# Kernel tuning notes

Measured on AMD Instinct MI355X. Metric: run time of the kernel, lower is better.

## Reference

```python
import jax, jax.numpy as jnp
import numpy as np

B, N, E, H, ET = 1, 50000, 600000, 128, 8
EPS = 1e-5


def setup_inputs() -> dict:
    key = jax.random.key(0)
    ks = jax.random.split(key, 20)
    s = 1.0 / np.sqrt(H)
    s2 = 1.0 / np.sqrt(2 * H)
    u = lambda k, shape, b: jax.random.uniform(k, shape, jnp.float32, -b, b)
    return {
        "hidden": jax.random.normal(ks[0], (B, N, H), jnp.float32),
        "edge_index": jax.random.randint(ks[1], (2, E), 0, N),
        "edge_type": jax.random.randint(ks[2], (E,), 0, ET),
        "edge_emb": jax.random.normal(ks[3], (ET, H), jnp.float32),
        "Wq": u(ks[4], (H, H), s), "bq": u(ks[5], (H,), s),
        "Wk": u(ks[6], (H, H), s), "bk": u(ks[7], (H,), s),
        "Wv": u(ks[8], (H, H), s), "bv": u(ks[9], (H,), s),
        "Web": u(ks[10], (H, 1), s), "beb": u(ks[11], (1,), s),
        "W1": u(ks[12], (2 * H, H), s2), "b1": u(ks[13], (H,), s2),
        "W2": u(ks[14], (H, H), s), "b2": u(ks[15], (H,), s),
        "gamma": jnp.ones((H,), jnp.float32),
        "beta": jnp.zeros((H,), jnp.float32),
    }


def reference(hidden, edge_index, edge_type, edge_emb, Wq, bq, Wk, bk, Wv, bv,
              Web, beb, W1, b1, W2, b2, gamma, beta):
    source, target = edge_index[0], edge_index[1]
    src_h = hidden[:, source]                      # [B,E,H] gather
    tgt_h = hidden[:, target]                      # [B,E,H] gather
    eh = edge_emb[edge_type]                       # [E,H]

    q = tgt_h @ Wq + bq                            # [B,E,H]
    sk = src_h + eh[None]                          # [B,E,H]
    k = sk @ Wk + bk
    v = sk @ Wv + bv

    logits = (q * k).sum(-1) / np.sqrt(H)          # [B,E]
    logits = logits + (eh @ Web + beb)[:, 0][None] # edge bias, same across batch

    # segment softmax over incoming edges per target node
    lt = logits.T                                  # [E,B]
    mx = jax.ops.segment_max(lt, target, num_segments=N)   # [N,B]
    ex = jnp.exp(lt - mx[target])
    sm = jax.ops.segment_sum(ex, target, num_segments=N)   # [N,B]
    w = (ex / sm[target]).T                        # [B,E]

    messages = v * w[..., None]                    # [B,E,H]
    agg = jax.ops.segment_sum(jnp.moveaxis(messages, 1, 0), target,
                              num_segments=N)      # [N,B,H]
    agg = jnp.moveaxis(agg, 0, 1)                  # [B,N,H]

    h = jnp.concatenate([hidden, agg], axis=-1)    # [B,N,2H]
    upd = jax.nn.silu(h @ W1 + b1) @ W2 + b2

    x = hidden + upd
    mu = x.mean(-1, keepdims=True)
    var = ((x - mu) ** 2).mean(-1, keepdims=True)
    return (x - mu) / jnp.sqrt(var + EPS) * gamma + beta
```

## Files before the change

### kernel.cpp

```cpp
#include <hip/hip_runtime.h>
#include <math.h>

#define NN 50000
#define NPAD 50048
#define NTILES 3128
#define NE 600000
#define H 128
#define ET 8
#define EPS 1e-5f
#define INVSQ 0.08838834764831845f

typedef __attribute__((ext_vector_type(8))) short bf16x8;
typedef __attribute__((ext_vector_type(8))) unsigned short u16x8;
typedef __attribute__((ext_vector_type(4))) float f32x4;

static __device__ inline float bf_lo(unsigned int w) { return __uint_as_float(w << 16); }
static __device__ inline float bf_hi(unsigned int w) { return __uint_as_float(w & 0xFFFF0000u); }
static __device__ inline float bfu(unsigned short v) {
  return __uint_as_float((unsigned int)v << 16);
}
static __device__ inline unsigned short f2bf(float f) {
  unsigned int u = __float_as_uint(f);
  return (unsigned short)((u + 0x7FFFu + ((u >> 16) & 1u)) >> 16);
}

#define PH_B 3125
#define PW_B 384
#define ET_B 8
#define HIST_B 2344

__global__ __launch_bounds__(256) void prep_all_kernel(
    const float* __restrict__ hidden, const float* __restrict__ edge_emb,
    const float* __restrict__ Wq, const float* __restrict__ Wk, const float* __restrict__ Wv,
    const float* __restrict__ W1, const float* __restrict__ W2,
    const float* __restrict__ Web, const float* __restrict__ beb,
    const int* __restrict__ tgt,
    unsigned short* __restrict__ hcat, unsigned short* __restrict__ WqkvT,
    unsigned short* __restrict__ W1T, unsigned short* __restrict__ W2T,
    unsigned short* __restrict__ KefTT, float* __restrict__ Vef, float* __restrict__ ebuf,
    int* __restrict__ deg) {
  const int blk = blockIdx.x;
  const int t = threadIdx.x;
  if (blk < PH_B) {
    int g = blk * 256 + t;
    int row = g >> 4, seg = g & 15;
    const float4* src = (const float4*)(hidden + (size_t)row * 128 + seg * 8);
    float4 x0 = src[0], x1 = src[1];
    u16x8 o;
    o[0] = f2bf(x0.x); o[1] = f2bf(x0.y); o[2] = f2bf(x0.z); o[3] = f2bf(x0.w);
    o[4] = f2bf(x1.x); o[5] = f2bf(x1.y); o[6] = f2bf(x1.z); o[7] = f2bf(x1.w);
    *(u16x8*)(hcat + (size_t)row * 256 + seg * 8) = o;
  } else if (blk < PH_B + PW_B) {
    int idx = (blk - PH_B) * 256 + t;
    if (idx < 49152) {
      int r = idx >> 7, k = idx & 127;
      const float* W = (r < 128) ? Wq : (r < 256) ? Wk : Wv;
      WqkvT[idx] = f2bf(W[k * 128 + (r & 127)]);
    } else if (idx < 81920) {
      int j = idx - 49152;
      int r = j >> 8, k = j & 255;
      W1T[j] = f2bf(W1[k * 128 + r]);
    } else if (idx < 98304) {
      int j = idx - 81920;
      int r = j >> 7, k = j & 127;
      W2T[j] = f2bf(W2[k * 128 + r]);
    }
  } else if (blk < PH_B + PW_B + ET_B) {
    int e = blk - (PH_B + PW_B);
    if (t < 128) {
      float sk = 0.f, sv = 0.f;
      for (int i = 0; i < 128; ++i) {
        float ev = edge_emb[e * 128 + i];
        sk = fmaf(ev, Wk[i * 128 + t], sk);
        sv = fmaf(ev, Wv[i * 128 + t], sv);
      }
      KefTT[e * 128 + t] = f2bf(sk);
      KefTT[(e + 8) * 128 + t] = 0;
      Vef[e * 128 + t] = sv;
    } else if (t == 128) {
      float s2 = beb[0];
      for (int i = 0; i < 128; ++i) s2 = fmaf(edge_emb[e * 128 + i], Web[i], s2);
      ebuf[e] = s2;
    }
  } else {
    int e = (blk - (PH_B + PW_B + ET_B)) * 256 + t;
    if (e < NE) atomicAdd(&deg[tgt[e]], 1);
  }
}

__global__ __launch_bounds__(512) void qkv_mfma_kernel(
    const unsigned short* __restrict__ hcat, const unsigned short* __restrict__ WqkvT,
    const float* __restrict__ bq, const float* __restrict__ bk, const float* __restrict__ bv,
    const unsigned short* __restrict__ KefTT, const float* __restrict__ ebuf,
    unsigned short* __restrict__ Qb, unsigned short* __restrict__ KV_u16,
    float* __restrict__ qke) {
  __shared__ unsigned short stage[64][392];
  const int tid = threadIdx.x;
  const int w = tid >> 6, l = tid & 63;
  const int wr = w >> 2, wc = w & 3;
  const int lr = l & 15, lg = l >> 4;
  const int blk = blockIdx.x;

  f32x4 acc[2][6] = {};
  const unsigned short* Ab = hcat + (size_t)(blk * 64 + wr * 32 + lr) * 256 + lg * 8;
  const unsigned short* Bb = WqkvT + (size_t)(wc * 96 + lr) * 128 + lg * 8;
#pragma unroll
  for (int ks = 0; ks < 4; ++ks) {
    bf16x8 a0 = *(const bf16x8*)(Ab + ks * 32);
    bf16x8 a1 = *(const bf16x8*)(Ab + 16 * 256 + ks * 32);
#pragma unroll
    for (int ct = 0; ct < 6; ++ct) {
      bf16x8 b = *(const bf16x8*)(Bb + ct * 16 * 128 + ks * 32);
      acc[0][ct] = __builtin_amdgcn_mfma_f32_16x16x32_bf16(a0, b, acc[0][ct], 0, 0, 0);
      acc[1][ct] = __builtin_amdgcn_mfma_f32_16x16x32_bf16(a1, b, acc[1][ct], 0, 0, 0);
    }
  }
#pragma unroll
  for (int ct = 0; ct < 6; ++ct) {
    int c = wc * 96 + ct * 16 + lr;
    float bias = (c < 128) ? bq[c] : (c < 256) ? bk[c - 128] : bv[c - 256];
    float sc = (c < 128) ? INVSQ : 1.f;
    int off;
    if (c < 128) off = c;
    else if (c < 256) { int j = c - 128; off = 128 + ((j >> 1) << 2) + (j & 1); }
    else { int j = c - 256; off = 128 + ((j >> 1) << 2) + 2 + (j & 1); }
#pragma unroll
    for (int mt = 0; mt < 2; ++mt)
#pragma unroll
      for (int j = 0; j < 4; ++j)
        stage[wr * 32 + mt * 16 + lg * 4 + j][off] = f2bf((acc[mt][ct][j] + bias) * sc);
  }
  __syncthreads();
  for (int idx = tid; idx < 64 * 48; idx += 512) {
    int r = idx / 48, g = idx % 48;
    int row = blk * 64 + r;
    if (row >= NN) continue;
    u16x8 v = *(const u16x8*)(&stage[r][g * 8]);
    if (g < 16) *(u16x8*)(Qb + (size_t)row * 128 + g * 8) = v;
    else *(u16x8*)(KV_u16 + (size_t)row * 256 + (g - 16) * 8) = v;
  }
  if (w < 4) {
    f32x4 aq = {0.f, 0.f, 0.f, 0.f};
    const unsigned short* qrow = &stage[w * 16 + lr][0];
    const unsigned short* brow = KefTT + lr * 128;
#pragma unroll
    for (int ks = 0; ks < 4; ++ks) {
      bf16x8 af = *(const bf16x8*)(qrow + lg * 8 + ks * 32);
      bf16x8 bf = *(const bf16x8*)(brow + lg * 8 + ks * 32);
      aq = __builtin_amdgcn_mfma_f32_16x16x32_bf16(af, bf, aq, 0, 0, 0);
    }
    if (lr < 8) {
      float ebv = ebuf[lr];
#pragma unroll
      for (int j = 0; j < 4; ++j) {
        int node = blk * 64 + w * 16 + lg * 4 + j;
        if (node < NN) qke[(size_t)node * 8 + lr] = aq[j] + ebv;
      }
    }
  }
}

__global__ __launch_bounds__(256) void scan1_kernel(const int* __restrict__ deg,
                                                    int* __restrict__ excl,
                                                    int* __restrict__ sums) {
  __shared__ int buf[256];
  int idx = blockIdx.x * 256 + threadIdx.x;
  int v = (idx < NN) ? deg[idx] : 0;
  buf[threadIdx.x] = v;
  __syncthreads();
  for (int o = 1; o < 256; o <<= 1) {
    int tv = (threadIdx.x >= o) ? buf[threadIdx.x - o] : 0;
    __syncthreads();
    buf[threadIdx.x] += tv;
    __syncthreads();
  }
  if (idx < NN) excl[idx] = buf[threadIdx.x] - v;
  if (threadIdx.x == 255) sums[blockIdx.x] = buf[255];
}

__global__ __launch_bounds__(256) void scan2_kernel(int* __restrict__ sums, int nb) {
  __shared__ int buf[256];
  int v = (threadIdx.x < nb) ? sums[threadIdx.x] : 0;
  buf[threadIdx.x] = v;
  __syncthreads();
  for (int o = 1; o < 256; o <<= 1) {
    int tv = (threadIdx.x >= o) ? buf[threadIdx.x - o] : 0;
    __syncthreads();
    buf[threadIdx.x] += tv;
    __syncthreads();
  }
  if (threadIdx.x < nb) sums[threadIdx.x] = buf[threadIdx.x] - v;
}

__global__ __launch_bounds__(256) void scan3_kernel(const int* __restrict__ excl,
                                                    const int* __restrict__ sums,
                                                    int* __restrict__ row_off,
                                                    int* __restrict__ cursor) {
  int idx = blockIdx.x * 256 + threadIdx.x;
  if (idx < NN) {
    int r = excl[idx] + sums[blockIdx.x];
    row_off[idx] = r;
    cursor[idx] = r;
  }
  if (idx == 0) row_off[NN] = NE;
}

__global__ void scatter_kernel(const int* __restrict__ src, const int* __restrict__ tgt,
                               const int* __restrict__ et, int* __restrict__ cursor,
                               int* __restrict__ packed) {
  int e = blockIdx.x * blockDim.x + threadIdx.x;
  if (e < NE) {
    int pos = atomicAdd(&cursor[tgt[e]], 1);
    packed[pos] = src[e] | (et[e] << 16);
  }
}

__global__ __launch_bounds__(256) void attn_kernel(
    const unsigned short* __restrict__ Qb, const uint4* __restrict__ KV4,
    const float* __restrict__ qke, const float* __restrict__ Vef,
    const int* __restrict__ row_off, const int* __restrict__ packed,
    unsigned short* __restrict__ hcat_u16) {
  const int wid = (blockIdx.x * blockDim.x + threadIdx.x) >> 6;
  const int lane = threadIdx.x & 63;
  const int g = lane >> 4, m = lane & 15;
  const int beg = row_off[wid], end = row_off[wid + 1];
  u16x8 qv = *(const u16x8*)(Qb + (size_t)wid * 128 + m * 8);
  float q[8];
#pragma unroll
  for (int j = 0; j < 8; ++j) q[j] = bfu(qv[j]);
  const float* qkb = qke + (size_t)wid * 8;
  float a[8] = {0.f, 0.f, 0.f, 0.f, 0.f, 0.f, 0.f, 0.f};
  float s = 0.f;
  for (int i = beg; i < end; i += 8) {
    int iA = i + g, iB = i + 4 + g;
    bool vA = iA < end, vB = iB < end;
    int pA = packed[vA ? iA : beg];
    int pB = packed[vB ? iB : beg];
    int sA = pA & 0xFFFF, eA = pA >> 16;
    int sB = pB & 0xFFFF, eB = pB >> 16;
    const uint4* rowA = KV4 + (size_t)sA * 32 + m * 2;
    const uint4* rowB = KV4 + (size_t)sB * 32 + m * 2;
    uint4 xA0 = rowA[0], xA1 = rowA[1];
    uint4 xB0 = rowB[0], xB1 = rowB[1];
    float dA, dB;
    dA = bf_lo(xA0.x) * q[0];
    dB = bf_lo(xB0.x) * q[0];
    dA = fmaf(bf_hi(xA0.x), q[1], dA);
    dB = fmaf(bf_hi(xB0.x), q[1], dB);
    dA = fmaf(bf_lo(xA0.z), q[2], dA);
    dB = fmaf(bf_lo(xB0.z), q[2], dB);
    dA = fmaf(bf_hi(xA0.z), q[3], dA);
    dB = fmaf(bf_hi(xB0.z), q[3], dB);
    dA = fmaf(bf_lo(xA1.x), q[4], dA);
    dB = fmaf(bf_lo(xB1.x), q[4], dB);
    dA = fmaf(bf_hi(xA1.x), q[5], dA);
    dB = fmaf(bf_hi(xB1.x), q[5], dB);
    dA = fmaf(bf_lo(xA1.z), q[6], dA);
    dB = fmaf(bf_lo(xB1.z), q[6], dB);
    dA = fmaf(bf_hi(xA1.z), q[7], dA);
    dB = fmaf(bf_hi(xB1.z), q[7], dB);
#pragma unroll
    for (int o = 8; o >= 1; o >>= 1) {
      dA += __shfl_xor(dA, o);
      dB += __shfl_xor(dB, o);
    }
    float peA = __expf(dA + qkb[eA]);
    float peB = __expf(dB + qkb[eB]);
    peA = vA ? peA : 0.f;
    peB = vB ? peB : 0.f;
    s += peA + peB;
    const float4* vefA = (const float4*)(Vef + eA * 128 + m * 8);
    const float4* vefB = (const float4*)(Vef + eB * 128 + m * 8);
    float4 vA0 = vefA[0], vA1 = vefA[1];
    float4 vB0 = vefB[0], vB1 = vefB[1];
    a[0] = fmaf(peA, bf_lo(xA0.y) + vA0.x, a[0]);
    a[1] = fmaf(peA, bf_hi(xA0.y) + vA0.y, a[1]);
    a[2] = fmaf(peA, bf_lo(xA0.w) + vA0.z, a[2]);
    a[3] = fmaf(peA, bf_hi(xA0.w) + vA0.w, a[3]);
    a[4] = fmaf(peA, bf_lo(xA1.y) + vA1.x, a[4]);
    a[5] = fmaf(peA, bf_hi(xA1.y) + vA1.y, a[5]);
    a[6] = fmaf(peA, bf_lo(xA1.w) + vA1.z, a[6]);
    a[7] = fmaf(peA, bf_hi(xA1.w) + vA1.w, a[7]);
    a[0] = fmaf(peB, bf_lo(xB0.y) + vB0.x, a[0]);
    a[1] = fmaf(peB, bf_hi(xB0.y) + vB0.y, a[1]);
    a[2] = fmaf(peB, bf_lo(xB0.w) + vB0.z, a[2]);
    a[3] = fmaf(peB, bf_hi(xB0.w) + vB0.w, a[3]);
    a[4] = fmaf(peB, bf_lo(xB1.y) + vB1.x, a[4]);
    a[5] = fmaf(peB, bf_hi(xB1.y) + vB1.y, a[5]);
    a[6] = fmaf(peB, bf_lo(xB1.w) + vB1.z, a[6]);
    a[7] = fmaf(peB, bf_hi(xB1.w) + vB1.w, a[7]);
  }
#pragma unroll
  for (int o = 16; o <= 32; o <<= 1) {
    s += __shfl_xor(s, o);
#pragma unroll
    for (int j = 0; j < 8; ++j) a[j] += __shfl_xor(a[j], o);
  }
  if (g == 0) {
    float inv = (s > 0.f) ? 1.f / s : 0.f;
    u16x8 o;
#pragma unroll
    for (int j = 0; j < 8; ++j) o[j] = f2bf(a[j] * inv);
    *(u16x8*)(hcat_u16 + (size_t)wid * 256 + 128 + m * 8) = o;
  }
}

__global__ __launch_bounds__(512) void ffn_mfma_kernel(
    const unsigned short* __restrict__ hcat, const float* __restrict__ hidden,
    const unsigned short* __restrict__ W1T, const unsigned short* __restrict__ W2T,
    const float* __restrict__ b1, const float* __restrict__ b2,
    const float* __restrict__ gamma, const float* __restrict__ beta,
    float* __restrict__ out) {
  __shared__ unsigned short w1s[32768];
  __shared__ unsigned short w2s[16384];
  __shared__ unsigned short mids[8][2176];
  const int tid = threadIdx.x;
  const int w = tid >> 6, l = tid & 63;
  const int lr = l & 15, lg = l >> 4;

#pragma unroll
  for (int it = 0; it < 8; ++it) {
    int idx = it * 512 + tid;
    int c = idx >> 5, ks8 = idx & 31;
    u16x8 v = *(const u16x8*)(W1T + c * 256 + ks8 * 8);
    int byte = (c * 512 + ks8 * 16) ^ ((c & 7) << 4);
    *(u16x8*)((char*)w1s + byte) = v;
  }
#pragma unroll
  for (int it = 0; it < 4; ++it) {
    int idx = it * 512 + tid;
    int c = idx >> 4, ks8 = idx & 15;
    u16x8 v = *(const u16x8*)(W2T + c * 128 + ks8 * 8);
    int byte = (c * 256 + ks8 * 16) ^ ((c & 7) << 4);
    *(u16x8*)((char*)w2s + byte) = v;
  }
  __syncthreads();

  float bias1[8], bias2[8], ga[8], be[8];
#pragma unroll
  for (int ct = 0; ct < 8; ++ct) {
    int c = ct * 16 + lr;
    bias1[ct] = b1[c];
    bias2[ct] = b2[c];
    ga[ct] = gamma[c];
    be[ct] = beta[c];
  }
  unsigned short* midw = mids[w];
  const char* w1b = (const char*)w1s;
  const char* w2b = (const char*)w2s;

  for (int t = blockIdx.x * 8 + w; t < NTILES; t += 2048) {
    const unsigned short* Ab = hcat + (size_t)(t * 16 + lr) * 256 + lg * 8;
    bf16x8 a[8];
#pragma unroll
    for (int ks = 0; ks < 8; ++ks) a[ks] = *(const bf16x8*)(Ab + ks * 32);

    f32x4 acc[8] = {};
#pragma unroll
    for (int ks = 0; ks < 8; ++ks) {
#pragma unroll
      for (int ct = 0; ct < 8; ++ct) {
        int byte = ((ct * 16 + lr) * 512 + (lg * 8 + ks * 32) * 2) ^ ((lr & 7) << 4);
        bf16x8 b = *(const bf16x8*)(w1b + byte);
        acc[ct] = __builtin_amdgcn_mfma_f32_16x16x32_bf16(a[ks], b, acc[ct], 0, 0, 0);
      }
    }

    float res[8][4];
#pragma unroll
    for (int ct = 0; ct < 8; ++ct)
#pragma unroll
      for (int j = 0; j < 4; ++j) {
        int r = t * 16 + lg * 4 + j;
        res[ct][j] = (r < NN) ? hidden[(size_t)r * 128 + ct * 16 + lr] : 0.f;
      }

#pragma unroll
    for (int ct = 0; ct < 8; ++ct) {
      float bb = bias1[ct];
#pragma unroll
      for (int j = 0; j < 4; ++j) {
        float x = acc[ct][j] + bb;
        float sl = x / (1.f + __expf(-x));
        midw[(lg * 4 + j) * 136 + ct * 16 + lr] = f2bf(sl);
      }
    }
    asm volatile("s_waitcnt lgkmcnt(0)" ::: "memory");
    __builtin_amdgcn_sched_barrier(0);

    f32x4 acc2[8] = {};
#pragma unroll
    for (int ks = 0; ks < 4; ++ks) {
      bf16x8 a2 = *(const bf16x8*)(midw + lr * 136 + lg * 8 + ks * 32);
#pragma unroll
      for (int ct = 0; ct < 8; ++ct) {
        int byte = ((ct * 16 + lr) * 256 + (lg * 8 + ks * 32) * 2) ^ ((lr & 7) << 4);
        bf16x8 b = *(const bf16x8*)(w2b + byte);
        acc2[ct] = __builtin_amdgcn_mfma_f32_16x16x32_bf16(a2, b, acc2[ct], 0, 0, 0);
      }
    }

    float x[8][4];
#pragma unroll
    for (int ct = 0; ct < 8; ++ct)
#pragma unroll
      for (int j = 0; j < 4; ++j) x[ct][j] = acc2[ct][j] + bias2[ct] + res[ct][j];
#pragma unroll
    for (int j = 0; j < 4; ++j) {
      float s = 0.f, ss = 0.f;
#pragma unroll
      for (int ct = 0; ct < 8; ++ct) {
        s += x[ct][j];
        ss += x[ct][j] * x[ct][j];
      }
#pragma unroll
      for (int o = 8; o >= 1; o >>= 1) {
        s += __shfl_xor(s, o);
        ss += __shfl_xor(ss, o);
      }
      float mu = s * (1.f / 128.f);
      float inv = rsqrtf(ss * (1.f / 128.f) - mu * mu + EPS);
      int r = t * 16 + lg * 4 + j;
      if (r < NN) {
#pragma unroll
        for (int ct = 0; ct < 8; ++ct) {
          int c = ct * 16 + lr;
          out[(size_t)r * 128 + c] = (x[ct][j] - mu) * inv * ga[ct] + be[ct];
        }
      }
    }
  }
}

extern "C" void kernel_launch(void* const* d_in, const int* in_sizes, int n_in,
                              void* d_out, int out_size, void* d_ws, size_t ws_size,
                              hipStream_t stream) {
  const float* hidden = (const float*)d_in[0];
  const int* edge_index = (const int*)d_in[1];
  const int* edge_type = (const int*)d_in[2];
  const float* edge_emb = (const float*)d_in[3];
  const float* Wq = (const float*)d_in[4];
  const float* bq = (const float*)d_in[5];
  const float* Wk = (const float*)d_in[6];
  const float* bk = (const float*)d_in[7];
  const float* Wv = (const float*)d_in[8];
  const float* bv = (const float*)d_in[9];
  const float* Web = (const float*)d_in[10];
  const float* beb = (const float*)d_in[11];
  const float* W1 = (const float*)d_in[12];
  const float* b1 = (const float*)d_in[13];
  const float* W2 = (const float*)d_in[14];
  const float* b2 = (const float*)d_in[15];
  const float* gamma = (const float*)d_in[16];
  const float* beta = (const float*)d_in[17];
  float* out = (float*)d_out;

  const int* srcp = edge_index;
  const int* tgtp = edge_index + NE;

  size_t off = 0;
  auto alloc = [&](size_t bytes) {
    void* p = (char*)d_ws + off;
    off += (bytes + 255) & ~(size_t)255;
    return p;
  };
  unsigned short* hcat = (unsigned short*)alloc((size_t)NPAD * 256 * 2);
  unsigned short* Qb = (unsigned short*)alloc((size_t)NPAD * 128 * 2);
  unsigned short* KV = (unsigned short*)alloc((size_t)NPAD * 256 * 2);
  unsigned short* WqkvT = (unsigned short*)alloc(384 * 128 * 2);
  unsigned short* W1T = (unsigned short*)alloc(128 * 256 * 2);
  unsigned short* W2T = (unsigned short*)alloc(128 * 128 * 2);
  unsigned short* KefTT = (unsigned short*)alloc(16 * 128 * 2);
  float* Vef = (float*)alloc(ET * H * 4);
  float* ebuf = (float*)alloc(ET * 4);
  float* qke = (float*)alloc((size_t)NN * 8 * 4);
  int* deg = (int*)alloc((size_t)NN * 4);
  int* excl = (int*)alloc((size_t)NN * 4);
  int* sums = (int*)alloc(256 * 4);
  int* row_off = (int*)alloc((size_t)(NN + 1) * 4);
  int* cursor = (int*)alloc((size_t)NN * 4);
  int* packed = (int*)alloc((size_t)NE * 4);

  hipMemsetAsync(deg, 0, (size_t)NN * 4, stream);

  const int scan_blocks = (NN + 255) / 256;

  prep_all_kernel<<<PH_B + PW_B + ET_B + HIST_B, 256, 0, stream>>>(
      hidden, edge_emb, Wq, Wk, Wv, W1, W2, Web, beb, tgtp, hcat, WqkvT, W1T, W2T, KefTT, Vef,
      ebuf, deg);
  scan1_kernel<<<scan_blocks, 256, 0, stream>>>(deg, excl, sums);
  scan2_kernel<<<1, 256, 0, stream>>>(sums, scan_blocks);
  scan3_kernel<<<scan_blocks, 256, 0, stream>>>(excl, sums, row_off, cursor);
  scatter_kernel<<<(NE + 255) / 256, 256, 0, stream>>>(srcp, tgtp, edge_type, cursor, packed);
  qkv_mfma_kernel<<<NPAD / 64, 512, 0, stream>>>(hcat, WqkvT, bq, bk, bv, KefTT, ebuf, Qb, KV,
                                                 qke);
  attn_kernel<<<(NN * 64) / 256, 256, 0, stream>>>(Qb, (const uint4*)KV, qke, Vef, row_off,
                                                   packed, hcat);
  ffn_mfma_kernel<<<256, 512, 0, stream>>>(hcat, hidden, W1T, W2T, b1, b2, gamma, beta, out);
}
```

Before: 283.3 us.

## Fuse edge scatter into QKV kernel and factor edge-type V term out of attention loop

The CSR scatter is merged into the QKV MFMA launch as extra blocks, removing one kernel launch and letting the atomic scatter overlap with the matmul blocks. In the attention loop, the per-edge load of the edge-type V contribution (Vef) is replaced by accumulating softmax weight per edge type in lanes 0-7 of each group. The 8 type vectors are then applied once after the loop. This cuts per-edge memory traffic and FMAs, at the cost of extra select/shuffle work and some imbalance between QKV and scatter blocks.

```diff
diff --git a/kernel.cpp b/kernel.cpp
--- a/kernel.cpp
+++ b/kernel.cpp
@@ -9,6 +9,9 @@
 #define ET 8
 #define EPS 1e-5f
 #define INVSQ 0.08838834764831845f
+
+#define QKV_B 782
+#define SCAT_B 1172
 
 typedef __attribute__((ext_vector_type(8))) short bf16x8;
 typedef __attribute__((ext_vector_type(8))) unsigned short u16x8;
@@ -88,18 +91,30 @@
   }
 }
 
-__global__ __launch_bounds__(512) void qkv_mfma_kernel(
+__global__ __launch_bounds__(512) void qkv_scatter_kernel(
     const unsigned short* __restrict__ hcat, const unsigned short* __restrict__ WqkvT,
     const float* __restrict__ bq, const float* __restrict__ bk, const float* __restrict__ bv,
     const unsigned short* __restrict__ KefTT, const float* __restrict__ ebuf,
+    const int* __restrict__ srcp, const int* __restrict__ tgtp, const int* __restrict__ etyp,
+    int* __restrict__ cursor, int* __restrict__ packed,
     unsigned short* __restrict__ Qb, unsigned short* __restrict__ KV_u16,
     float* __restrict__ qke) {
   __shared__ unsigned short stage[64][392];
   const int tid = threadIdx.x;
+  const int blk = blockIdx.x;
+
+  if (blk >= QKV_B) {
+    int e = (blk - QKV_B) * 512 + tid;
+    if (e < NE) {
+      int pos = atomicAdd(&cursor[tgtp[e]], 1);
+      packed[pos] = srcp[e] | (etyp[e] << 16);
+    }
+    return;
+  }
+
   const int w = tid >> 6, l = tid & 63;
   const int wr = w >> 2, wc = w & 3;
   const int lr = l & 15, lg = l >> 4;
-  const int blk = blockIdx.x;
 
   f32x4 acc[2][6] = {};
   const unsigned short* Ab = hcat + (size_t)(blk * 64 + wr * 32 + lr) * 256 + lg * 8;
@@ -205,16 +220,6 @@
   if (idx == 0) row_off[NN] = NE;
 }
 
-__global__ void scatter_kernel(const int* __restrict__ src, const int* __restrict__ tgt,
-                               const int* __restrict__ et, int* __restrict__ cursor,
-                               int* __restrict__ packed) {
-  int e = blockIdx.x * blockDim.x + threadIdx.x;
-  if (e < NE) {
-    int pos = atomicAdd(&cursor[tgt[e]], 1);
-    packed[pos] = src[e] | (et[e] << 16);
-  }
-}
-
 __global__ __launch_bounds__(256) void attn_kernel(
     const unsigned short* __restrict__ Qb, const uint4* __restrict__ KV4,
     const float* __restrict__ qke, const float* __restrict__ Vef,
@@ -229,8 +234,9 @@
 #pragma unroll
   for (int j = 0; j < 8; ++j) q[j] = bfu(qv[j]);
   const float* qkb = qke + (size_t)wid * 8;
+  const bool mlt8 = (m < 8);
   float a[8] = {0.f, 0.f, 0.f, 0.f, 0.f, 0.f, 0.f, 0.f};
-  float s = 0.f;
+  float s = 0.f, se = 0.f;
   for (int i = beg; i < end; i += 8) {
     int iA = i + g, iB = i + 4 + g;
     bool vA = iA < end, vB = iB < end;
@@ -269,32 +275,45 @@
     peA = vA ? peA : 0.f;
     peB = vB ? peB : 0.f;
     s += peA + peB;
-    const float4* vefA = (const float4*)(Vef + eA * 128 + m * 8);
-    const float4* vefB = (const float4*)(Vef + eB * 128 + m * 8);
-    float4 vA0 = vefA[0], vA1 = vefA[1];
-    float4 vB0 = vefB[0], vB1 = vefB[1];
-    a[0] = fmaf(peA, bf_lo(xA0.y) + vA0.x, a[0]);
-    a[1] = fmaf(peA, bf_hi(xA0.y) + vA0.y, a[1]);
-    a[2] = fmaf(peA, bf_lo(xA0.w) + vA0.z, a[2]);
-    a[3] = fmaf(peA, bf_hi(xA0.w) + vA0.w, a[3]);
-    a[4] = fmaf(peA, bf_lo(xA1.y) + vA1.x, a[4]);
-    a[5] = fmaf(peA, bf_hi(xA1.y) + vA1.y, a[5]);
-    a[6] = fmaf(peA, bf_lo(xA1.w) + vA1.z, a[6]);
-    a[7] = fmaf(peA, bf_hi(xA1.w) + vA1.w, a[7]);
-    a[0] = fmaf(peB, bf_lo(xB0.y) + vB0.x, a[0]);
-    a[1] = fmaf(peB, bf_hi(xB0.y) + vB0.y, a[1]);
-    a[2] = fmaf(peB, bf_lo(xB0.w) + vB0.z, a[2]);
-    a[3] = fmaf(peB, bf_hi(xB0.w) + vB0.w, a[3]);
-    a[4] = fmaf(peB, bf_lo(xB1.y) + vB1.x, a[4]);
-    a[5] = fmaf(peB, bf_hi(xB1.y) + vB1.y, a[5]);
-    a[6] = fmaf(peB, bf_lo(xB1.w) + vB1.z, a[6]);
-    a[7] = fmaf(peB, bf_hi(xB1.w) + vB1.w, a[7]);
+    se += (mlt8 && eA == m) ? peA : 0.f;
+    se += (mlt8 && eB == m) ? peB : 0.f;
+    a[0] = fmaf(peA, bf_lo(xA0.y), a[0]);
+    a[1] = fmaf(peA, bf_hi(xA0.y), a[1]);
+    a[2] = fmaf(peA, bf_lo(xA0.w), a[2]);
+    a[3] = fmaf(peA, bf_hi(xA0.w), a[3]);
+    a[4] = fmaf(peA, bf_lo(xA1.y), a[4]);
+    a[5] = fmaf(peA, bf_hi(xA1.y), a[5]);
+    a[6] = fmaf(peA, bf_lo(xA1.w), a[6]);
+    a[7] = fmaf(peA, bf_hi(xA1.w), a[7]);
+    a[0] = fmaf(peB, bf_lo(xB0.y), a[0]);
+    a[1] = fmaf(peB, bf_hi(xB0.y), a[1]);
+    a[2] = fmaf(peB, bf_lo(xB0.w), a[2]);
+    a[3] = fmaf(peB, bf_hi(xB0.w), a[3]);
+    a[4] = fmaf(peB, bf_lo(xB1.y), a[4]);
+    a[5] = fmaf(peB, bf_hi(xB1.y), a[5]);
+    a[6] = fmaf(peB, bf_lo(xB1.w), a[6]);
+    a[7] = fmaf(peB, bf_hi(xB1.w), a[7]);
   }
 #pragma unroll
   for (int o = 16; o <= 32; o <<= 1) {
     s += __shfl_xor(s, o);
+    se += __shfl_xor(se, o);
 #pragma unroll
     for (int j = 0; j < 8; ++j) a[j] += __shfl_xor(a[j], o);
+  }
+#pragma unroll
+  for (int t = 0; t < 8; ++t) {
+    float st = __shfl(se, (lane & 48) | t);
+    const float4* vf = (const float4*)(Vef + t * 128 + m * 8);
+    float4 v0 = vf[0], v1 = vf[1];
+    a[0] = fmaf(st, v0.x, a[0]);
+    a[1] = fmaf(st, v0.y, a[1]);
+    a[2] = fmaf(st, v0.z, a[2]);
+    a[3] = fmaf(st, v0.w, a[3]);
+    a[4] = fmaf(st, v1.x, a[4]);
+    a[5] = fmaf(st, v1.y, a[5]);
+    a[6] = fmaf(st, v1.z, a[6]);
+    a[7] = fmaf(st, v1.w, a[7]);
   }
   if (g == 0) {
     float inv = (s > 0.f) ? 1.f / s : 0.f;
@@ -491,9 +510,8 @@
   scan1_kernel<<<scan_blocks, 256, 0, stream>>>(deg, excl, sums);
   scan2_kernel<<<1, 256, 0, stream>>>(sums, scan_blocks);
   scan3_kernel<<<scan_blocks, 256, 0, stream>>>(excl, sums, row_off, cursor);
-  scatter_kernel<<<(NE + 255) / 256, 256, 0, stream>>>(srcp, tgtp, edge_type, cursor, packed);
-  qkv_mfma_kernel<<<NPAD / 64, 512, 0, stream>>>(hcat, WqkvT, bq, bk, bv, KefTT, ebuf, Qb, KV,
-                                                 qke);
+  qkv_scatter_kernel<<<QKV_B + SCAT_B, 512, 0, stream>>>(
+      hcat, WqkvT, bq, bk, bv, KefTT, ebuf, srcp, tgtp, edge_type, cursor, packed, Qb, KV, qke);
   attn_kernel<<<(NN * 64) / 256, 256, 0, stream>>>(Qb, (const uint4*)KV, qke, Vef, row_off,
                                                    packed, hcat);
   ffn_mfma_kernel<<<256, 512, 0, stream>>>(hcat, hidden, W1T, W2T, b1, b2, gamma, beta, out);
```

Measured after the change: 273.8 us. -3.4%, faster.
